# Optimization experiments

Measured on AMD Instinct MI355X. Metric: run time of the kernel, lower is better.

Reference implementation:

```python
import jax, jax.numpy as jnp
import numpy as np

B, L, H = 16, 512, 1024
K_START, K_END = 5, 5
LN_EPS = 1e-12
NEG = 1e30


def _layer_norm(x, gamma, beta):
    mu = jnp.mean(x, axis=-1, keepdims=True)
    var = jnp.mean(jnp.square(x - mu), axis=-1, keepdims=True)
    return (x - mu) * jax.lax.rsqrt(var + LN_EPS) * gamma + beta


def setup_inputs() -> dict:
    key = jax.random.key(0)
    ks = jax.random.split(key, 10)
    s = 0.02
    sequence_data = jax.random.normal(ks[0], (B, L, H), jnp.float32)
    class_index = jax.random.randint(ks[1], (B,), 0, L, dtype=jnp.int32)
    paragraph_mask = (jax.random.uniform(ks[2], (B, L)) > 0.1).astype(jnp.float32)
    paragraph_mask = paragraph_mask.at[:, 0].set(1.0)  # guarantee >=1 valid position per row
    return {
        'sequence_data': sequence_data,
        'class_index': class_index,
        'paragraph_mask': paragraph_mask,
        'W_start': jax.random.normal(ks[3], (H, 1), jnp.float32) * s,
        'b_start': jnp.zeros((1,), jnp.float32),
        'W_end_in': jax.random.normal(ks[4], (2 * H, H), jnp.float32) * s,
        'b_end_in': jnp.zeros((H,), jnp.float32),
        'ln_gamma': jnp.ones((H,), jnp.float32),
        'ln_beta': jnp.zeros((H,), jnp.float32),
        'W_end_out': jax.random.normal(ks[5], (H, 1), jnp.float32) * s,
        'b_end_out': jnp.zeros((1,), jnp.float32),
        'W_ans_in': jax.random.normal(ks[6], (2 * H, H), jnp.float32) * s,
        'b_ans_in': jnp.zeros((H,), jnp.float32),
        'W_ans_out': jax.random.normal(ks[7], (H, 1), jnp.float32) * s,
    }


def reference(sequence_data, class_index, paragraph_mask,
              W_start, b_start, W_end_in, b_end_in, ln_gamma, ln_beta,
              W_end_out, b_end_out, W_ans_in, b_ans_in, W_ans_out):
    mask = paragraph_mask  # [b, l] float, 1 = valid

    # ---- start logits ----
    start_logits = jnp.einsum('blh,ho->bl', sequence_data, W_start) + b_start[0]  # [b,l]
    masked_start_logits = start_logits * mask - NEG * (1.0 - mask)
    start_predictions = jax.nn.log_softmax(masked_start_logits, axis=-1)

    # ---- beam search over start positions (inference branch) ----
    start_top_predictions, start_top_index = jax.lax.top_k(start_predictions, K_START)  # [b,k]
    # one-hot einsum gather 'blh,bkl->bkh' expressed as direct indexing
    start_features = jnp.take_along_axis(sequence_data, start_top_index[:, :, None], axis=1)  # [b,k,h]

    # end_logits inner dense on concat([tiled seq, tiled start_features]) along h:
    # split the [2h, h] kernel and broadcast-add instead of materializing the tiled concat.
    W1, W2 = W_end_in[:H], W_end_in[H:]
    inner = jnp.tanh(
        jnp.einsum('blh,hd->bld', sequence_data, W1)[:, :, None, :]
        + jnp.einsum('bkh,hd->bkd', start_features, W2)[:, None, :, :]
        + b_end_in
    )  # [b,l,k,h]
    inner = _layer_norm(inner, ln_gamma, ln_beta)
    end_logits = jnp.einsum('blkh,ho->blk', inner, W_end_out) + b_end_out[0]  # [b,l,k]
    end_logits = jnp.transpose(end_logits, (0, 2, 1))  # [b,k,l]

    mask_k = mask[:, None, :]  # [b,1,l]
    masked_end_logits = end_logits * mask_k - NEG * (1.0 - mask_k)
    end_predictions = jax.nn.log_softmax(masked_end_logits, axis=-1)

    end_top_predictions, _end_top_index = jax.lax.top_k(end_predictions, K_END)  # [b,k,k2]
    end_top_predictions = end_top_predictions.reshape(-1, K_START * K_END)

    # ---- answer (class) logits ----
    class_feature = sequence_data[jnp.arange(sequence_data.shape[0]), class_index]  # [b,h]
    start_p = jax.nn.softmax(masked_start_logits, axis=-1)
    start_feature = jnp.einsum('blh,bl->bh', sequence_data, start_p)
    answer_feature = jnp.concatenate([start_feature, class_feature], axis=-1)  # [b,2h]
    answer_feature = jnp.tanh(answer_feature @ W_ans_in + b_ans_in)  # dropout is identity at inference
    class_logits = (answer_feature @ W_ans_out)[:, 0]  # [b]

    return (start_predictions, end_predictions, masked_start_logits, masked_end_logits,
            start_top_predictions, end_top_predictions, class_logits)
```

## Files before the change

kernel.cpp:

```cpp
#include <hip/hip_runtime.h>
#include <math.h>

#define HD   1024
#define LSEQ 512
#define NB   16
#define KTOP 5
#define NEGV 1e30f

typedef __bf16 bf16x8 __attribute__((ext_vector_type(8)));
typedef float  f32x4  __attribute__((ext_vector_type(4)));

__device__ inline unsigned short f2bf(float f) {
  unsigned u = __float_as_uint(f);
  unsigned r = (u + 0x7FFFu + ((u >> 16) & 1u)) >> 16;
  return (unsigned short)r;
}
__device__ inline float bf2f(unsigned short u) {
  return __uint_as_float(((unsigned)u) << 16);
}

__device__ inline float fast_tanh(float x) {
  float e = __expf(-2.f * fabsf(x));
  float v = (1.f - e) / (1.f + e);
  return copysignf(v, x);
}

__device__ inline float tanh_scaled(float xs) {
  float e = __builtin_amdgcn_exp2f(xs);
  float r = __builtin_amdgcn_rcpf(1.f + e);
  return fmaf(-2.f, r, 1.f);
}

#define GLDS(g, l) __builtin_amdgcn_global_load_lds(                      \
    (const __attribute__((address_space(1))) unsigned int*)(g),          \
    (__attribute__((address_space(3))) unsigned int*)(l), 16, 0, 0)


__device__ __forceinline__ void sm_body(int row, const float* __restrict__ xin,
                                        float* __restrict__ lsm_out,
                                        float* __restrict__ top_out,
                                        float* __restrict__ p_out,
                                        int* __restrict__ idx_out) {
  __shared__ float redf[4];
  __shared__ int redi[4];
  __shared__ float bc_m, bc_s;
  __shared__ int bc_i;
  int t = threadIdx.x, lane = t & 63, wid = t >> 6;
  const float* x = xin + (size_t)row * LSEQ;
  float x0 = x[t], x1 = x[t + 256];

  float m = fmaxf(x0, x1);
#pragma unroll
  for (int off = 32; off; off >>= 1) m = fmaxf(m, __shfl_xor(m, off));
  if (lane == 0) redf[wid] = m;
  __syncthreads();
  if (t == 0) bc_m = fmaxf(fmaxf(redf[0], redf[1]), fmaxf(redf[2], redf[3]));
  __syncthreads();
  m = bc_m;

  float e0 = expf(x0 - m), e1 = expf(x1 - m);
  float s = e0 + e1;
#pragma unroll
  for (int off = 32; off; off >>= 1) s += __shfl_xor(s, off);
  if (lane == 0) redf[wid] = s;
  __syncthreads();
  if (t == 0) bc_s = redf[0] + redf[1] + redf[2] + redf[3];
  __syncthreads();
  s = bc_s;
  float ls = logf(s);

  lsm_out[(size_t)row * LSEQ + t] = x0 - m - ls;
  lsm_out[(size_t)row * LSEQ + t + 256] = x1 - m - ls;
  if (p_out) {
    float inv = 1.f / s;
    p_out[(size_t)row * LSEQ + t] = e0 * inv;
    p_out[(size_t)row * LSEQ + t + 256] = e1 * inv;
  }

  bool a0 = true, a1 = true;
  for (int it = 0; it < KTOP; ++it) {
    float v0 = a0 ? x0 : -INFINITY;
    float v1 = a1 ? x1 : -INFINITY;
    float bv = v0; int bi = t;
    if (v1 > bv) { bv = v1; bi = t + 256; }
#pragma unroll
    for (int off = 32; off; off >>= 1) {
      float ov = __shfl_xor(bv, off);
      int oi = __shfl_xor(bi, off);
      if (ov > bv || (ov == bv && oi < bi)) { bv = ov; bi = oi; }
    }
    __syncthreads();
    if (lane == 0) { redf[wid] = bv; redi[wid] = bi; }
    __syncthreads();
    if (t == 0) {
      float wv = redf[0]; int wi = redi[0];
      for (int w = 1; w < 4; ++w)
        if (redf[w] > wv || (redf[w] == wv && redi[w] < wi)) { wv = redf[w]; wi = redi[w]; }
      top_out[row * KTOP + it] = wv - m - ls;
      if (idx_out) idx_out[row * KTOP + it] = wi;
      bc_i = wi;
    }
    __syncthreads();
    int wi = bc_i;
    if (wi == t) a0 = false;
    if (wi == t + 256) a1 = false;
  }
}

__device__ __forceinline__ void gemm_body(int gid,
                                          const unsigned short* __restrict__ Abf,
                                          const unsigned short* __restrict__ Bt,
                                          unsigned short* __restrict__ X1) {
  __shared__ unsigned short SH[32768];
  unsigned short* As = SH;
  unsigned short* Bs = SH + 16384;
  int t = threadIdx.x;
  int w = t >> 6, lane = t & 63, ln = lane & 15, hi = lane >> 4;
  int wr = w >> 1, wc = w & 1;
  int R0 = (gid >> 3) * 128, C0 = (gid & 7) * 128;

  f32x4 acc[4][4] = {};

#define STAGE(buf, kc)                                                        \
  do {                                                                        \
    _Pragma("unroll")                                                         \
    for (int p_ = 0; p_ < 4; ++p_) {                                          \
      int rr_ = p_ * 32 + (t >> 3);                                           \
      int cc_ = (t & 7) ^ (rr_ & 7);                                          \
      GLDS(Abf + (size_t)(R0 + rr_) * HD + (kc) + cc_ * 8,                    \
           As + (buf) * 8192 + p_ * 2048 + w * 512);                          \
      GLDS(Bt + (size_t)(C0 + rr_) * HD + (kc) + cc_ * 8,                     \
           Bs + (buf) * 8192 + p_ * 2048 + w * 512);                          \
    }                                                                         \
  } while (0)

  STAGE(0, 0);
  for (int it = 0; it < 16; ++it) {
    int cur = it & 1;
    if (it < 15) {
      STAGE(cur ^ 1, (it + 1) * 64);
      asm volatile("s_waitcnt vmcnt(8)" ::: "memory");
    } else {
      asm volatile("s_waitcnt vmcnt(0)" ::: "memory");
    }
    __builtin_amdgcn_s_barrier();
    __builtin_amdgcn_sched_barrier(0);
#pragma unroll
    for (int ks = 0; ks < 2; ++ks) {
      bf16x8 av[4], bv[4];
#pragma unroll
      for (int m = 0; m < 4; ++m) {
        int r = wr * 64 + m * 16 + ln;
        av[m] = *(const bf16x8*)(const void*)&As[cur * 8192 + r * 64 + (((ks * 4 + hi) ^ (r & 7)) * 8)];
      }
#pragma unroll
      for (int n = 0; n < 4; ++n) {
        int r = wc * 64 + n * 16 + ln;
        bv[n] = *(const bf16x8*)(const void*)&Bs[cur * 8192 + r * 64 + (((ks * 4 + hi) ^ (r & 7)) * 8)];
      }
#pragma unroll
      for (int m = 0; m < 4; ++m)
#pragma unroll
        for (int n = 0; n < 4; ++n)
          acc[m][n] = __builtin_amdgcn_mfma_f32_16x16x32_bf16(av[m], bv[n], acc[m][n], 0, 0, 0);
    }
    __builtin_amdgcn_sched_barrier(0);
    __builtin_amdgcn_s_barrier();
  }
#undef STAGE

#pragma unroll
  for (int m = 0; m < 4; ++m)
#pragma unroll
    for (int j = 0; j < 4; ++j) {
      int row = R0 + wr * 64 + m * 16 + hi * 4 + j;
#pragma unroll
      for (int n = 0; n < 4; ++n) {
        int col = C0 + wc * 64 + n * 16 + ln;
        X1[(size_t)row * HD + col] = f2bf(acc[m][n][j]);
      }
    }
}

__device__ __forceinline__ void x2slice_body(int q, const float* __restrict__ seq,
                                             const int* __restrict__ idx,
                                             const float* __restrict__ Wei,
                                             float* __restrict__ x2p) {
  __shared__ float srow[128];
  int bk = q >> 3, s = q & 7, t = threadIdx.x;
  int b = bk / KTOP;
  int l = idx[bk];
  if (t < 128) srow[t] = seq[((size_t)(b * LSEQ + l)) * HD + s * 128 + t];
  __syncthreads();
  const float* W2 = Wei + (size_t)HD * HD + (size_t)s * 128 * HD;
  float4 acc = make_float4(0.f, 0.f, 0.f, 0.f);
#pragma unroll 8
  for (int h = 0; h < 128; ++h) {
    float4 wv = *(const float4*)(W2 + (size_t)h * HD + 4 * t);
    float sv = srow[h];
    acc.x = fmaf(sv, wv.x, acc.x);
    acc.y = fmaf(sv, wv.y, acc.y);
    acc.z = fmaf(sv, wv.z, acc.z);
    acc.w = fmaf(sv, wv.w, acc.w);
  }
  float* dst = x2p + (size_t)bk * HD + 4 * t;
  atomicAdd(dst + 0, acc.x);
  atomicAdd(dst + 1, acc.y);
  atomicAdd(dst + 2, acc.z);
  atomicAdd(dst + 3, acc.w);
}

__device__ __forceinline__ void ansin_body(int q, const float* __restrict__ seq,
                                           const float* __restrict__ p_ws,
                                           const int* __restrict__ cls,
                                           float* __restrict__ pa,
                                           float* __restrict__ cf) {
  __shared__ float ps[16];
  int b = q >> 5, s = q & 31, t = threadIdx.x;
  if (t < 16) ps[t] = p_ws[b * LSEQ + s * 16 + t];
  __syncthreads();
  const float* sb = seq + (size_t)(b * LSEQ + s * 16) * HD;
  float4 acc = make_float4(0.f, 0.f, 0.f, 0.f);
#pragma unroll
  for (int r = 0; r < 16; ++r) {
    float4 v = *(const float4*)(sb + (size_t)r * HD + 4 * t);
    float p = ps[r];
    acc.x = fmaf(p, v.x, acc.x);
    acc.y = fmaf(p, v.y, acc.y);
    acc.z = fmaf(p, v.z, acc.z);
    acc.w = fmaf(p, v.w, acc.w);
  }
  *(float4*)(pa + ((size_t)b * 32 + s) * HD + 4 * t) = acc;
  if (s == 0) {
    int ci = cls[b];
    *(float4*)(cf + (size_t)b * HD + 4 * t) =
        *(const float4*)(seq + (size_t)(b * LSEQ + ci) * HD + 4 * t);
  }
}

__device__ __forceinline__ void endrow_body(int bx, const unsigned short* __restrict__ X1,
                                            const float* __restrict__ x2p,
                                            const float* __restrict__ gw_ws,
                                            const float* __restrict__ sgb_ws,
                                            const float* __restrict__ mask,
                                            float* __restrict__ mel) {
  __shared__ float x2s[KTOP * HD];
  const float A = 2.885390081777927f;
  int t = threadIdx.x, wave = t >> 6, lane = t & 63;
  int row = bx * 4 + wave;
  int b = row >> 9, l = row & 511;

  {
    const float4* src = (const float4*)(x2p + (size_t)b * KTOP * HD);
    float4* dst = (float4*)x2s;
    for (int i = t; i < KTOP * HD / 4; i += 256) {
      float4 v = src[i];
      dst[i] = make_float4(v.x * A, v.y * A, v.z * A, v.w * A);
    }
  }

  float xs[16], gwr[16];
  const unsigned short* xrow = X1 + (size_t)row * HD + lane * 4;
#pragma unroll
  for (int q = 0; q < 4; ++q) {
    ushort4 u = *(const ushort4*)(xrow + q * 256);
    xs[4 * q + 0] = bf2f(u.x) * A;
    xs[4 * q + 1] = bf2f(u.y) * A;
    xs[4 * q + 2] = bf2f(u.z) * A;
    xs[4 * q + 3] = bf2f(u.w) * A;
    float4 g = *(const float4*)(gw_ws + q * 256 + lane * 4);
    gwr[4 * q + 0] = g.x; gwr[4 * q + 1] = g.y;
    gwr[4 * q + 2] = g.z; gwr[4 * q + 3] = g.w;
  }
  float mv = mask[row];
  float sG = sgb_ws[0], sBW = sgb_ws[1];
  __syncthreads();

#pragma unroll
  for (int k = 0; k < KTOP; ++k) {
    float sv = 0.f, s2 = 0.f, sg = 0.f;
#pragma unroll
    for (int q = 0; q < 4; ++q) {
      float4 xq = *(const float4*)&x2s[k * HD + q * 256 + lane * 4];
      float v0 = tanh_scaled(xs[4 * q + 0] + xq.x);
      float v1 = tanh_scaled(xs[4 * q + 1] + xq.y);
      float v2 = tanh_scaled(xs[4 * q + 2] + xq.z);
      float v3 = tanh_scaled(xs[4 * q + 3] + xq.w);
      sv += v0 + v1 + v2 + v3;
      s2 = fmaf(v0, v0, s2); s2 = fmaf(v1, v1, s2);
      s2 = fmaf(v2, v2, s2); s2 = fmaf(v3, v3, s2);
      sg = fmaf(v0, gwr[4 * q + 0], sg); sg = fmaf(v1, gwr[4 * q + 1], sg);
      sg = fmaf(v2, gwr[4 * q + 2], sg); sg = fmaf(v3, gwr[4 * q + 3], sg);
    }
#pragma unroll
    for (int off = 32; off; off >>= 1) {
      sv += __shfl_xor(sv, off);
      s2 += __shfl_xor(s2, off);
      sg += __shfl_xor(sg, off);
    }
    if (lane == 0) {
      float mu = sv * (1.f / (float)HD);
      float var = s2 * (1.f / (float)HD) - mu * mu;
      float rr = rsqrtf(var + 1e-12f);
      float logit = rr * (sg - mu * sG) + sBW;
      mel[((size_t)b * KTOP + k) * LSEQ + l] = logit * mv - NEGV * (1.f - mv);
    }
  }
}

__device__ __forceinline__ void ansmid_body(int q, const float* __restrict__ pa,
                                            const float* __restrict__ cf,
                                            const float* __restrict__ Wai,
                                            float* __restrict__ pans) {
  __shared__ float a_s[128];
  int b = q >> 4, c = q & 15, t = threadIdx.x;
  if (t < 128) {
    int i = c * 128 + t;
    float av;
    if (i < HD) {
      av = 0.f;
#pragma unroll
      for (int s = 0; s < 32; ++s) av += pa[((size_t)b * 32 + s) * HD + i];
    } else {
      av = cf[(size_t)b * HD + (i - HD)];
    }
    a_s[t] = av;
  }
  __syncthreads();
  float4 acc = make_float4(0.f, 0.f, 0.f, 0.f);
#pragma unroll 8
  for (int r = 0; r < 128; ++r) {
    float4 wv = *(const float4*)(Wai + (size_t)(c * 128 + r) * HD + 4 * t);
    float a = a_s[r];
    acc.x = fmaf(a, wv.x, acc.x);
    acc.y = fmaf(a, wv.y, acc.y);
    acc.z = fmaf(a, wv.z, acc.z);
    acc.w = fmaf(a, wv.w, acc.w);
  }
  *(float4*)(pans + ((size_t)b * 16 + c) * HD + 4 * t) = acc;
}

__device__ __forceinline__ void ansfinal_body(int b, const float* __restrict__ pans,
                                              const float* __restrict__ bai,
                                              const float* __restrict__ Wao,
                                              float* __restrict__ out6) {
  __shared__ float red[4];
  int t = threadIdx.x, lane = t & 63, wid = t >> 6;
  float4 a = *(const float4*)(bai + 4 * t);
#pragma unroll
  for (int c = 0; c < 16; ++c) {
    float4 p = *(const float4*)(pans + ((size_t)b * 16 + c) * HD + 4 * t);
    a.x += p.x; a.y += p.y; a.z += p.z; a.w += p.w;
  }
  float4 wo = *(const float4*)(Wao + 4 * t);
  float part = fast_tanh(a.x) * wo.x + fast_tanh(a.y) * wo.y +
               fast_tanh(a.z) * wo.z + fast_tanh(a.w) * wo.w;
#pragma unroll
  for (int off = 32; off; off >>= 1) part += __shfl_xor(part, off);
  if (lane == 0) red[wid] = part;
  __syncthreads();
  if (t == 0) out6[b] = red[0] + red[1] + red[2] + red[3];
}


__global__ void k_prep(const float* __restrict__ seq,
                       unsigned short* __restrict__ seqb,
                       const float* __restrict__ Wst,
                       const float* __restrict__ bst,
                       const float* __restrict__ mask,
                       float* __restrict__ msl,
                       const float* __restrict__ Wei,
                       unsigned short* __restrict__ w1t,
                       const float* __restrict__ gam,
                       const float* __restrict__ bet,
                       const float* __restrict__ Weo,
                       const float* __restrict__ beo,
                       float* __restrict__ gw_ws,
                       float* __restrict__ sgb_ws,
                       const float* __restrict__ bei,
                       float* __restrict__ x2p) {
  __shared__ unsigned short tile[32][33];
  __shared__ float redp[4][2];
  int bx = blockIdx.x;
  if (bx < 2048) {
    int wave = threadIdx.x >> 6, lane = threadIdx.x & 63;
    int row = bx * 4 + wave;
    const float4* s4 = (const float4*)(seq + (size_t)row * HD);
    const float4* w4 = (const float4*)Wst;
    ushort4* o4 = (ushort4*)(seqb + (size_t)row * HD);
    float acc = 0.f;
#pragma unroll
    for (int m = 0; m < 4; ++m) {
      int i = lane + 64 * m;
      float4 a = s4[i], w = w4[i];
      acc += a.x * w.x + a.y * w.y + a.z * w.z + a.w * w.w;
      ushort4 o;
      o.x = f2bf(a.x); o.y = f2bf(a.y); o.z = f2bf(a.z); o.w = f2bf(a.w);
      o4[i] = o;
    }
#pragma unroll
    for (int off = 32; off; off >>= 1) acc += __shfl_xor(acc, off);
    if (lane == 0) {
      float logit = acc + bst[0];
      float mv = mask[row];
      msl[row] = logit * mv - NEGV * (1.f - mv);
    }
  } else if (bx < 3072) {
    int tb = bx - 2048;
    int h0 = (tb & 31) * 32, d0 = (tb >> 5) * 32;
    int tx = threadIdx.x & 31, ty = threadIdx.x >> 5;
#pragma unroll
    for (int i = 0; i < 4; ++i)
      tile[ty + 8 * i][tx] = f2bf(Wei[(size_t)(h0 + ty + 8 * i) * HD + d0 + tx]);
    __syncthreads();
#pragma unroll
    for (int i = 0; i < 4; ++i)
      w1t[(size_t)(d0 + ty + 8 * i) * HD + h0 + tx] = tile[tx][ty + 8 * i];
  } else if (bx == 3072) {
    int t = threadIdx.x, wave = t >> 6, lane = t & 63;
    float4 g = ((const float4*)gam)[t];
    float4 w = ((const float4*)Weo)[t];
    float4 bv = ((const float4*)bet)[t];
    float4 gwv = make_float4(g.x * w.x, g.y * w.y, g.z * w.z, g.w * w.w);
    ((float4*)gw_ws)[t] = gwv;
    float pg = gwv.x + gwv.y + gwv.z + gwv.w;
    float pb = bv.x * w.x + bv.y * w.y + bv.z * w.z + bv.w * w.w;
#pragma unroll
    for (int off = 32; off; off >>= 1) {
      pg += __shfl_xor(pg, off);
      pb += __shfl_xor(pb, off);
    }
    if (lane == 0) { redp[wave][0] = pg; redp[wave][1] = pb; }
    __syncthreads();
    if (t == 0) {
      sgb_ws[0] = redp[0][0] + redp[1][0] + redp[2][0] + redp[3][0];
      sgb_ws[1] = redp[0][1] + redp[1][1] + redp[2][1] + redp[3][1] + beo[0];
    }
  } else {
    int row = bx - 3073;
    ((float4*)(x2p + (size_t)row * HD))[threadIdx.x] = ((const float4*)bei)[threadIdx.x];
  }
}

__global__ void k_softmax_topk(const float* __restrict__ xin,
                               float* __restrict__ lsm_out,
                               float* __restrict__ top_out,
                               float* __restrict__ p_out,
                               int* __restrict__ idx_out) {
  sm_body(blockIdx.x, xin, lsm_out, top_out, p_out, idx_out);
}

__launch_bounds__(256, 2)
__global__ void k_big(const unsigned short* __restrict__ Abf,
                      const unsigned short* __restrict__ Bt,
                      unsigned short* __restrict__ X1,
                      const float* __restrict__ seq,
                      const int* __restrict__ idx,
                      const float* __restrict__ Wei,
                      float* __restrict__ x2p,
                      const float* __restrict__ p_ws,
                      const int* __restrict__ cls,
                      float* __restrict__ pa,
                      float* __restrict__ cf) {
  int id = blockIdx.x;
  int grp = id / 13, rem = id % 13;
  if (rem < 4) gemm_body(grp * 4 + rem, Abf, Bt, X1);
  else if (rem < 9) x2slice_body(grp * 5 + (rem - 4), seq, idx, Wei, x2p);
  else ansin_body(grp * 4 + (rem - 9), seq, p_ws, cls, pa, cf);
}

__global__ void k_end2(const unsigned short* __restrict__ X1,
                       const float* __restrict__ x2p,
                       const float* __restrict__ gw_ws,
                       const float* __restrict__ sgb_ws,
                       const float* __restrict__ mask,
                       float* __restrict__ mel,
                       const float* __restrict__ pa,
                       const float* __restrict__ cf,
                       const float* __restrict__ Wai,
                       float* __restrict__ pans) {
  int bx = blockIdx.x;
  if (bx < 2048) endrow_body(bx, X1, x2p, gw_ws, sgb_ws, mask, mel);
  else ansmid_body(bx - 2048, pa, cf, Wai, pans);
}

__global__ void k_fin(const float* __restrict__ mel,
                      float* __restrict__ lsm_out,
                      float* __restrict__ top_out,
                      const float* __restrict__ pans,
                      const float* __restrict__ bai,
                      const float* __restrict__ Wao,
                      float* __restrict__ out6) {
  int bx = blockIdx.x;
  if (bx < NB * KTOP) sm_body(bx, mel, lsm_out, top_out, nullptr, nullptr);
  else ansfinal_body(bx - NB * KTOP, pans, bai, Wao, out6);
}

__global__ void k_x2f(const float* __restrict__ seq, const int* __restrict__ idx,
                      const float* __restrict__ Wei, float* __restrict__ x2p) {
  x2slice_body(blockIdx.x, seq, idx, Wei, x2p);
}
__global__ void k_ansin_f(const float* __restrict__ seq, const float* __restrict__ p_ws,
                          const int* __restrict__ cls, float* __restrict__ pa,
                          float* __restrict__ cf) {
  ansin_body(blockIdx.x, seq, p_ws, cls, pa, cf);
}
__global__ void k_ansmid_f(const float* __restrict__ pa, const float* __restrict__ cf,
                           const float* __restrict__ Wai, float* __restrict__ pans) {
  ansmid_body(blockIdx.x, pa, cf, Wai, pans);
}

__launch_bounds__(256, 2)
__global__ void k_gemm_end_at(const unsigned short* __restrict__ Abf,
                              const unsigned short* __restrict__ Bt,
                              const float* __restrict__ x2p,
                              const float* __restrict__ gamma,
                              const float* __restrict__ Wout,
                              float* __restrict__ outp) {
  __shared__ unsigned short As[2][128 * 64];
  __shared__ unsigned short Bs[2][128 * 64];
  int t = threadIdx.x;
  int w = t >> 6, lane = t & 63, ln = lane & 15, hi = lane >> 4;
  int wr = w >> 1, wc = w & 1;
  int R0 = blockIdx.x * 128, C0 = blockIdx.y * 128;
  int b = R0 >> 9;
  f32x4 acc[4][4] = {};
#define STAGE(buf, kc)                                                        \
  do {                                                                        \
    _Pragma("unroll")                                                         \
    for (int p_ = 0; p_ < 4; ++p_) {                                          \
      int rr_ = p_ * 32 + (t >> 3);                                           \
      int cc_ = (t & 7) ^ (rr_ & 7);                                          \
      GLDS(Abf + (size_t)(R0 + rr_) * HD + (kc) + cc_ * 8,                    \
           &As[buf][p_ * 2048 + w * 512]);                                    \
      GLDS(Bt + (size_t)(C0 + rr_) * HD + (kc) + cc_ * 8,                     \
           &Bs[buf][p_ * 2048 + w * 512]);                                    \
    }                                                                         \
  } while (0)
  STAGE(0, 0);
  for (int it = 0; it < 16; ++it) {
    int cur = it & 1;
    if (it < 15) {
      STAGE(cur ^ 1, (it + 1) * 64);
      asm volatile("s_waitcnt vmcnt(8)" ::: "memory");
    } else {
      asm volatile("s_waitcnt vmcnt(0)" ::: "memory");
    }
    __builtin_amdgcn_s_barrier();
    __builtin_amdgcn_sched_barrier(0);
#pragma unroll
    for (int ks = 0; ks < 2; ++ks) {
      bf16x8 av[4], bv[4];
#pragma unroll
      for (int m = 0; m < 4; ++m) {
        int r = wr * 64 + m * 16 + ln;
        av[m] = *(const bf16x8*)(const void*)&As[cur][r * 64 + (((ks * 4 + hi) ^ (r & 7)) * 8)];
      }
#pragma unroll
      for (int n = 0; n < 4; ++n) {
        int r = wc * 64 + n * 16 + ln;
        bv[n] = *(const bf16x8*)(const void*)&Bs[cur][r * 64 + (((ks * 4 + hi) ^ (r & 7)) * 8)];
      }
#pragma unroll
      for (int m = 0; m < 4; ++m)
#pragma unroll
        for (int n = 0; n < 4; ++n)
          acc[m][n] = __builtin_amdgcn_mfma_f32_16x16x32_bf16(av[m], bv[n], acc[m][n], 0, 0, 0);
    }
    __builtin_amdgcn_sched_barrier(0);
    __builtin_amdgcn_s_barrier();
  }
#undef STAGE
  float gsv[4];
  float x2v[4][KTOP];
#pragma unroll
  for (int n = 0; n < 4; ++n) {
    int c = C0 + wc * 64 + n * 16 + ln;
    gsv[n] = gamma[c] * Wout[c];
#pragma unroll
    for (int k = 0; k < KTOP; ++k) x2v[n][k] = x2p[((size_t)b * KTOP + k) * HD + c];
  }
#pragma unroll
  for (int m = 0; m < 4; ++m)
#pragma unroll
    for (int j = 0; j < 4; ++j) {
      int row = R0 + wr * 64 + m * 16 + hi * 4 + j;
#pragma unroll
      for (int k = 0; k < KTOP; ++k) {
        float sv = 0.f, s2 = 0.f, sg = 0.f;
#pragma unroll
        for (int n = 0; n < 4; ++n) {
          float v = fast_tanh(acc[m][n][j] + x2v[n][k]);
          sv += v; s2 += v * v; sg += v * gsv[n];
        }
#pragma unroll
        for (int off = 8; off; off >>= 1) {
          sv += __shfl_xor(sv, off);
          s2 += __shfl_xor(s2, off);
          sg += __shfl_xor(sg, off);
        }
        if (ln == 0) {
          float* p = outp + ((size_t)row * KTOP + k) * 3;
          atomicAdd(p, sv);
          atomicAdd(p + 1, s2);
          atomicAdd(p + 2, sg);
        }
      }
    }
}

__global__ void k_end_final(const float* __restrict__ sums,
                            const float* __restrict__ gamma,
                            const float* __restrict__ beta,
                            const float* __restrict__ Wout,
                            const float* __restrict__ beo,
                            const float* __restrict__ mask,
                            float* __restrict__ mel) {
  int bk = blockIdx.x, b = bk / KTOP, k = bk % KTOP;
  int t = threadIdx.x, lane = t & 63, wid = t >> 6;
  __shared__ float red[4][2];
  float pg = 0.f, pb = 0.f;
  for (int i = t; i < HD; i += 256) {
    float wv = Wout[i];
    pg += gamma[i] * wv;
    pb += beta[i] * wv;
  }
#pragma unroll
  for (int off = 32; off; off >>= 1) {
    pg += __shfl_xor(pg, off);
    pb += __shfl_xor(pb, off);
  }
  if (lane == 0) { red[wid][0] = pg; red[wid][1] = pb; }
  __syncthreads();
  float sG = red[0][0] + red[1][0] + red[2][0] + red[3][0];
  float sBW = red[0][1] + red[1][1] + red[2][1] + red[3][1] + beo[0];
  for (int l = t; l < LSEQ; l += 256) {
    int row = b * LSEQ + l;
    const float* s = sums + ((size_t)row * KTOP + k) * 3;
    float sv = s[0], s2 = s[1], sg = s[2];
    float mu = sv * (1.f / (float)HD);
    float var = s2 * (1.f / (float)HD) - mu * mu;
    float rr = rsqrtf(var + 1e-12f);
    float logit = rr * (sg - mu * sG) + sBW;
    float mv = mask[row];
    mel[((size_t)b * KTOP + k) * LSEQ + l] = logit * mv - NEGV * (1.f - mv);
  }
}

extern "C" void kernel_launch(void* const* d_in, const int* in_sizes, int n_in,
                              void* d_out, int out_size, void* d_ws, size_t ws_size,
                              hipStream_t stream) {
  (void)in_sizes; (void)n_in; (void)out_size;
  const float* seq = (const float*)d_in[0];
  const int*   cls = (const int*)d_in[1];
  const float* mask = (const float*)d_in[2];
  const float* Wst = (const float*)d_in[3];
  const float* bst = (const float*)d_in[4];
  const float* Wei = (const float*)d_in[5];
  const float* bei = (const float*)d_in[6];
  const float* gam = (const float*)d_in[7];
  const float* bet = (const float*)d_in[8];
  const float* Weo = (const float*)d_in[9];
  const float* beo = (const float*)d_in[10];
  const float* Wai = (const float*)d_in[11];
  const float* bai = (const float*)d_in[12];
  const float* Wao = (const float*)d_in[13];

  float* out = (float*)d_out;
  float* out0 = out;
  float* out1 = out0 + 8192;
  float* out2 = out1 + 40960;
  float* out3 = out2 + 8192;
  float* out4 = out3 + 40960;
  float* out5 = out4 + 80;
  float* out6 = out5 + 400;

  char* p = (char*)d_ws;
  unsigned short* seqb = (unsigned short*)p;  p += (size_t)8192 * 1024 * 2;
  unsigned short* w1t  = (unsigned short*)p;  p += (size_t)1024 * 1024 * 2;
  float* p_ws   = (float*)p;                  p += 8192 * 4;
  int*   idx_ws = (int*)p;                    p += 128 * 4;
  float* x2p    = (float*)p;                  p += (size_t)80 * 1024 * 4;
  float* gw_ws  = (float*)p;                  p += 1024 * 4;
  float* sgb_ws = (float*)p;                  p += 4 * 4;
  float* pa     = (float*)p;                  p += (size_t)16 * 32 * 1024 * 4;
  float* cf     = (float*)p;                  p += (size_t)16 * 1024 * 4;
  float* pans   = (float*)p;                  p += (size_t)16 * 16 * 1024 * 4;
  unsigned short* x1 = (unsigned short*)p;
  float* sums = (float*)p;
  size_t base = (size_t)(p - (char*)d_ws);
  size_t need_big = base + (size_t)8192 * 1024 * 2;
  size_t need_small = base + (size_t)8192 * KTOP * 3 * 4;

  k_prep<<<3153, 256, 0, stream>>>(seq, seqb, Wst, bst, mask, out2, Wei, w1t,
                                   gam, bet, Weo, beo, gw_ws, sgb_ws, bei, x2p);
  k_softmax_topk<<<NB, 256, 0, stream>>>(out2, out0, out4, p_ws, idx_ws);

  if (ws_size >= need_big) {
    k_big<<<1664, 256, 0, stream>>>(seqb, w1t, x1, seq, idx_ws, Wei, x2p,
                                    p_ws, cls, pa, cf);
    k_end2<<<2304, 256, 0, stream>>>(x1, x2p, gw_ws, sgb_ws, mask, out3,
                                     pa, cf, Wai, pans);
  } else if (ws_size >= need_small) {
    k_x2f<<<640, 256, 0, stream>>>(seq, idx_ws, Wei, x2p);
    hipMemsetAsync(sums, 0, (size_t)8192 * KTOP * 3 * sizeof(float), stream);
    k_gemm_end_at<<<dim3(64, 8), 256, 0, stream>>>(seqb, w1t, x2p, gam, Weo, sums);
    k_end_final<<<NB * KTOP, 256, 0, stream>>>(sums, gam, bet, Weo, beo, mask, out3);
    k_ansin_f<<<512, 256, 0, stream>>>(seq, p_ws, cls, pa, cf);
    k_ansmid_f<<<256, 256, 0, stream>>>(pa, cf, Wai, pans);
  }

  k_fin<<<96, 256, 0, stream>>>(out3, out1, out5, pans, bai, Wao, out6);
}
```

Measured before the change: 95.94 us.

## Overlap softmax/top-k with main GEMM and compute beam features via MFMA GEMM

The softmax/top-k stage is folded into the first GEMM launch as 16 extra blocks, so the big seq×W1 GEMM no longer waits behind a separate 16-block kernel. The second half of W_end_in is now transposed to bf16 in the prep kernel. The beam-feature product is then computed with a bf16 MFMA tiled GEMM over gathered rows, replacing the fp32 atomicAdd slice kernel and the bias-init blocks. The trade-offs are an extra 2 MB bf16 weight buffer, bf16 precision on the gathered features, and an extra kernel launch.

Measured after the change: 88.71 us. 7.5% less time.

```diff
diff --git a/kernel.cpp b/kernel.cpp
--- a/kernel.cpp
+++ b/kernel.cpp
@@ -107,7 +107,7 @@
   }
 }
 
-__device__ __forceinline__ void gemm_body(int gid,
+__device__ __forceinline__ void gemm_body(int R0, int C0,
                                           const unsigned short* __restrict__ Abf,
                                           const unsigned short* __restrict__ Bt,
                                           unsigned short* __restrict__ X1) {
@@ -117,7 +117,6 @@
   int t = threadIdx.x;
   int w = t >> 6, lane = t & 63, ln = lane & 15, hi = lane >> 4;
   int wr = w >> 1, wc = w & 1;
-  int R0 = (gid >> 3) * 128, C0 = (gid & 7) * 128;
 
   f32x4 acc[4][4] = {};
 
@@ -182,32 +181,92 @@
     }
 }
 
-__device__ __forceinline__ void x2slice_body(int q, const float* __restrict__ seq,
-                                             const int* __restrict__ idx,
-                                             const float* __restrict__ Wei,
-                                             float* __restrict__ x2p) {
-  __shared__ float srow[128];
-  int bk = q >> 3, s = q & 7, t = threadIdx.x;
-  int b = bk / KTOP;
-  int l = idx[bk];
-  if (t < 128) srow[t] = seq[((size_t)(b * LSEQ + l)) * HD + s * 128 + t];
-  __syncthreads();
-  const float* W2 = Wei + (size_t)HD * HD + (size_t)s * 128 * HD;
-  float4 acc = make_float4(0.f, 0.f, 0.f, 0.f);
-#pragma unroll 8
-  for (int h = 0; h < 128; ++h) {
-    float4 wv = *(const float4*)(W2 + (size_t)h * HD + 4 * t);
-    float sv = srow[h];
-    acc.x = fmaf(sv, wv.x, acc.x);
-    acc.y = fmaf(sv, wv.y, acc.y);
-    acc.z = fmaf(sv, wv.z, acc.z);
-    acc.w = fmaf(sv, wv.w, acc.w);
-  }
-  float* dst = x2p + (size_t)bk * HD + 4 * t;
-  atomicAdd(dst + 0, acc.x);
-  atomicAdd(dst + 1, acc.y);
-  atomicAdd(dst + 2, acc.z);
-  atomicAdd(dst + 3, acc.w);
+__device__ __forceinline__ void x2gemm_body(int cid,
+                                            const unsigned short* __restrict__ seqb,
+                                            const unsigned short* __restrict__ w2t,
+                                            const int* __restrict__ idx,
+                                            const float* __restrict__ bei,
+                                            float* __restrict__ x2p) {
+  __shared__ unsigned short SH2[32768];
+  unsigned short* As = SH2;
+  unsigned short* Bs = SH2 + 16384;
+  int t = threadIdx.x;
+  int w = t >> 6, lane = t & 63, ln = lane & 15, hi = lane >> 4;
+  int wr = w >> 1, wc = w & 1;
+  int C0 = cid * 128;
+
+  size_t abase[4];
+#pragma unroll
+  for (int p_ = 0; p_ < 4; ++p_) {
+    int rr = p_ * 32 + (t >> 3);
+    int bk = rr < 80 ? rr : 0;
+    int l = idx[bk];
+    abase[p_] = ((size_t)((bk / KTOP) * LSEQ + l)) * HD;
+  }
+
+  f32x4 acc[4][4] = {};
+
+#define STAGE2(buf, kc)                                                       \
+  do {                                                                        \
+    _Pragma("unroll")                                                         \
+    for (int p_ = 0; p_ < 4; ++p_) {                                          \
+      int rr_ = p_ * 32 + (t >> 3);                                           \
+      int cc_ = (t & 7) ^ (rr_ & 7);                                          \
+      GLDS(seqb + abase[p_] + (kc) + cc_ * 8,                                 \
+           As + (buf) * 8192 + p_ * 2048 + w * 512);                          \
+      GLDS(w2t + (size_t)(C0 + rr_) * HD + (kc) + cc_ * 8,                    \
+           Bs + (buf) * 8192 + p_ * 2048 + w * 512);                          \
+    }                                                                         \
+  } while (0)
+
+  STAGE2(0, 0);
+  for (int it = 0; it < 16; ++it) {
+    int cur = it & 1;
+    if (it < 15) {
+      STAGE2(cur ^ 1, (it + 1) * 64);
+      asm volatile("s_waitcnt vmcnt(8)" ::: "memory");
+    } else {
+      asm volatile("s_waitcnt vmcnt(0)" ::: "memory");
+    }
+    __builtin_amdgcn_s_barrier();
+    __builtin_amdgcn_sched_barrier(0);
+#pragma unroll
+    for (int ks = 0; ks < 2; ++ks) {
+      bf16x8 av[4], bv[4];
+#pragma unroll
+      for (int m = 0; m < 4; ++m) {
+        int r = wr * 64 + m * 16 + ln;
+        av[m] = *(const bf16x8*)(const void*)&As[cur * 8192 + r * 64 + (((ks * 4 + hi) ^ (r & 7)) * 8)];
+      }
+#pragma unroll
+      for (int n = 0; n < 4; ++n) {
+        int r = wc * 64 + n * 16 + ln;
+        bv[n] = *(const bf16x8*)(const void*)&Bs[cur * 8192 + r * 64 + (((ks * 4 + hi) ^ (r & 7)) * 8)];
+      }
+#pragma unroll
+      for (int m = 0; m < 4; ++m)
+#pragma unroll
+        for (int n = 0; n < 4; ++n)
+          acc[m][n] = __builtin_amdgcn_mfma_f32_16x16x32_bf16(av[m], bv[n], acc[m][n], 0, 0, 0);
+    }
+    __builtin_amdgcn_sched_barrier(0);
+    __builtin_amdgcn_s_barrier();
+  }
+#undef STAGE2
+
+#pragma unroll
+  for (int m = 0; m < 4; ++m)
+#pragma unroll
+    for (int j = 0; j < 4; ++j) {
+      int row = wr * 64 + m * 16 + hi * 4 + j;
+      if (row < 80) {
+#pragma unroll
+        for (int n = 0; n < 4; ++n) {
+          int col = C0 + wc * 64 + n * 16 + ln;
+          x2p[(size_t)row * HD + col] = acc[m][n][j] + bei[col];
+        }
+      }
+    }
 }
 
 __device__ __forceinline__ void ansin_body(int q, const float* __restrict__ seq,
@@ -371,14 +430,13 @@
                        float* __restrict__ msl,
                        const float* __restrict__ Wei,
                        unsigned short* __restrict__ w1t,
+                       unsigned short* __restrict__ w2t,
                        const float* __restrict__ gam,
                        const float* __restrict__ bet,
                        const float* __restrict__ Weo,
                        const float* __restrict__ beo,
                        float* __restrict__ gw_ws,
-                       float* __restrict__ sgb_ws,
-                       const float* __restrict__ bei,
-                       float* __restrict__ x2p) {
+                       float* __restrict__ sgb_ws) {
   __shared__ unsigned short tile[32][33];
   __shared__ float redp[4][2];
   int bx = blockIdx.x;
@@ -405,18 +463,21 @@
       float mv = mask[row];
       msl[row] = logit * mv - NEGV * (1.f - mv);
     }
-  } else if (bx < 3072) {
+  } else if (bx < 4096) {
     int tb = bx - 2048;
-    int h0 = (tb & 31) * 32, d0 = (tb >> 5) * 32;
+    const float* Wsrc = Wei + (tb >= 1024 ? (size_t)HD * HD : 0);
+    unsigned short* Wdst = (tb >= 1024) ? w2t : w1t;
+    int tb2 = tb & 1023;
+    int h0 = (tb2 & 31) * 32, d0 = (tb2 >> 5) * 32;
     int tx = threadIdx.x & 31, ty = threadIdx.x >> 5;
 #pragma unroll
     for (int i = 0; i < 4; ++i)
-      tile[ty + 8 * i][tx] = f2bf(Wei[(size_t)(h0 + ty + 8 * i) * HD + d0 + tx]);
+      tile[ty + 8 * i][tx] = f2bf(Wsrc[(size_t)(h0 + ty + 8 * i) * HD + d0 + tx]);
     __syncthreads();
 #pragma unroll
     for (int i = 0; i < 4; ++i)
-      w1t[(size_t)(d0 + ty + 8 * i) * HD + h0 + tx] = tile[tx][ty + 8 * i];
-  } else if (bx == 3072) {
+      Wdst[(size_t)(d0 + ty + 8 * i) * HD + h0 + tx] = tile[tx][ty + 8 * i];
+  } else {
     int t = threadIdx.x, wave = t >> 6, lane = t & 63;
     float4 g = ((const float4*)gam)[t];
     float4 w = ((const float4*)Weo)[t];
@@ -436,9 +497,6 @@
       sgb_ws[0] = redp[0][0] + redp[1][0] + redp[2][0] + redp[3][0];
       sgb_ws[1] = redp[0][1] + redp[1][1] + redp[2][1] + redp[3][1] + beo[0];
     }
-  } else {
-    int row = bx - 3073;
-    ((float4*)(x2p + (size_t)row * HD))[threadIdx.x] = ((const float4*)bei)[threadIdx.x];
   }
 }
 
@@ -451,22 +509,37 @@
 }
 
 __launch_bounds__(256, 2)
-__global__ void k_big(const unsigned short* __restrict__ Abf,
+__global__ void k_gsm(const unsigned short* __restrict__ Abf,
                       const unsigned short* __restrict__ Bt,
                       unsigned short* __restrict__ X1,
+                      const float* __restrict__ msl,
+                      float* __restrict__ lsm_out,
+                      float* __restrict__ top_out,
+                      float* __restrict__ p_out,
+                      int* __restrict__ idx_out) {
+  int id = blockIdx.x;
+  if (id < 16) {
+    sm_body(id, msl, lsm_out, top_out, p_out, idx_out);
+  } else {
+    int gid = id - 16;
+    gemm_body((gid & 63) * 128, (gid >> 6) * 128, Abf, Bt, X1);
+  }
+}
+
+__launch_bounds__(256, 2)
+__global__ void k_x2a(const unsigned short* __restrict__ seqb,
+                      const unsigned short* __restrict__ w2t,
+                      const int* __restrict__ idx,
+                      const float* __restrict__ bei,
+                      float* __restrict__ x2p,
                       const float* __restrict__ seq,
-                      const int* __restrict__ idx,
-                      const float* __restrict__ Wei,
-                      float* __restrict__ x2p,
                       const float* __restrict__ p_ws,
                       const int* __restrict__ cls,
                       float* __restrict__ pa,
                       float* __restrict__ cf) {
   int id = blockIdx.x;
-  int grp = id / 13, rem = id % 13;
-  if (rem < 4) gemm_body(grp * 4 + rem, Abf, Bt, X1);
-  else if (rem < 9) x2slice_body(grp * 5 + (rem - 4), seq, idx, Wei, x2p);
-  else ansin_body(grp * 4 + (rem - 9), seq, p_ws, cls, pa, cf);
+  if (id < 8) x2gemm_body(id, seqb, w2t, idx, bei, x2p);
+  else ansin_body(id - 8, seq, p_ws, cls, pa, cf);
 }
 
 __global__ void k_end2(const unsigned short* __restrict__ X1,
@@ -496,10 +569,37 @@
   else ansfinal_body(bx - NB * KTOP, pans, bai, Wao, out6);
 }
 
+__global__ void k_x2init(const float* __restrict__ bei, float* __restrict__ x2p) {
+  ((float4*)(x2p + (size_t)blockIdx.x * HD))[threadIdx.x] = ((const float4*)bei)[threadIdx.x];
+}
+
 __global__ void k_x2f(const float* __restrict__ seq, const int* __restrict__ idx,
                       const float* __restrict__ Wei, float* __restrict__ x2p) {
-  x2slice_body(blockIdx.x, seq, idx, Wei, x2p);
-}
+  __shared__ float srow[128];
+  int q = blockIdx.x;
+  int bk = q >> 3, s = q & 7, t = threadIdx.x;
+  int b = bk / KTOP;
+  int l = idx[bk];
+  if (t < 128) srow[t] = seq[((size_t)(b * LSEQ + l)) * HD + s * 128 + t];
+  __syncthreads();
+  const float* W2 = Wei + (size_t)HD * HD + (size_t)s * 128 * HD;
+  float4 acc = make_float4(0.f, 0.f, 0.f, 0.f);
+#pragma unroll 8
+  for (int h = 0; h < 128; ++h) {
+    float4 wv = *(const float4*)(W2 + (size_t)h * HD + 4 * t);
+    float sv = srow[h];
+    acc.x = fmaf(sv, wv.x, acc.x);
+    acc.y = fmaf(sv, wv.y, acc.y);
+    acc.z = fmaf(sv, wv.z, acc.z);
+    acc.w = fmaf(sv, wv.w, acc.w);
+  }
+  float* dst = x2p + (size_t)bk * HD + 4 * t;
+  atomicAdd(dst + 0, acc.x);
+  atomicAdd(dst + 1, acc.y);
+  atomicAdd(dst + 2, acc.z);
+  atomicAdd(dst + 3, acc.w);
+}
+
 __global__ void k_ansin_f(const float* __restrict__ seq, const float* __restrict__ p_ws,
                           const int* __restrict__ cls, float* __restrict__ pa,
                           float* __restrict__ cf) {
@@ -678,6 +778,7 @@
   char* p = (char*)d_ws;
   unsigned short* seqb = (unsigned short*)p;  p += (size_t)8192 * 1024 * 2;
   unsigned short* w1t  = (unsigned short*)p;  p += (size_t)1024 * 1024 * 2;
+  unsigned short* w2t  = (unsigned short*)p;  p += (size_t)1024 * 1024 * 2;
   float* p_ws   = (float*)p;                  p += 8192 * 4;
   int*   idx_ws = (int*)p;                    p += 128 * 4;
   float* x2p    = (float*)p;                  p += (size_t)80 * 1024 * 4;
@@ -692,16 +793,18 @@
   size_t need_big = base + (size_t)8192 * 1024 * 2;
   size_t need_small = base + (size_t)8192 * KTOP * 3 * 4;
 
-  k_prep<<<3153, 256, 0, stream>>>(seq, seqb, Wst, bst, mask, out2, Wei, w1t,
-                                   gam, bet, Weo, beo, gw_ws, sgb_ws, bei, x2p);
-  k_softmax_topk<<<NB, 256, 0, stream>>>(out2, out0, out4, p_ws, idx_ws);
+  k_prep<<<4097, 256, 0, stream>>>(seq, seqb, Wst, bst, mask, out2, Wei, w1t, w2t,
+                                   gam, bet, Weo, beo, gw_ws, sgb_ws);
 
   if (ws_size >= need_big) {
-    k_big<<<1664, 256, 0, stream>>>(seqb, w1t, x1, seq, idx_ws, Wei, x2p,
-                                    p_ws, cls, pa, cf);
+    k_gsm<<<528, 256, 0, stream>>>(seqb, w1t, x1, out2, out0, out4, p_ws, idx_ws);
+    k_x2a<<<520, 256, 0, stream>>>(seqb, w2t, idx_ws, bei, x2p,
+                                   seq, p_ws, cls, pa, cf);
     k_end2<<<2304, 256, 0, stream>>>(x1, x2p, gw_ws, sgb_ws, mask, out3,
                                      pa, cf, Wai, pans);
   } else if (ws_size >= need_small) {
+    k_softmax_topk<<<NB, 256, 0, stream>>>(out2, out0, out4, p_ws, idx_ws);
+    k_x2init<<<80, 256, 0, stream>>>(bei, x2p);
     k_x2f<<<640, 256, 0, stream>>>(seq, idx_ws, Wei, x2p);
     hipMemsetAsync(sums, 0, (size_t)8192 * KTOP * 3 * sizeof(float), stream);
     k_gemm_end_at<<<dim3(64, 8), 256, 0, stream>>>(seqb, w1t, x2p, gam, Weo, sums);
```
